# Performance work log

Measured on AMD Instinct MI355X. Metric: run time of the kernel, lower is better.

Reference implementation:

```python
import jax, jax.numpy as jnp
import numpy as np
from jax import lax

# Dims (match init_kwargs)
NP, DP = 32, 8      # num_primary_a, dim_primary_a
NT, DT = 16, 16     # num_timecaps_a, dim_timecaps
KT = 3              # kernel_timecaps_a
EPS = 1e-7


def setup_inputs() -> dict:
    key = jax.random.key(0)
    k1, k2, k3 = jax.random.split(key, 3)
    B, T = 8, 1024
    x = jax.random.normal(k1, (B, T, NP, DP), dtype=jnp.float32)
    # Conv2D kernel: HWIO = [kernel_t, dim_primary_a, in_ch=1, out_ch=NT*DT]
    conv_kernel = jax.random.normal(k2, (KT, DP, 1, NT * DT), dtype=jnp.float32) * 0.05
    conv_bias = jnp.zeros((NT * DT,), dtype=jnp.float32)
    B_weight = jax.random.normal(k3, (T, NT, 1, NP), dtype=jnp.float32) * 0.05
    return {"x": x, "conv_kernel": conv_kernel, "conv_bias": conv_bias, "B_weight": B_weight}


def reference(x, conv_kernel, conv_bias, B_weight):
    B, T, Np, Dp = x.shape
    # reshape1: [B, T, Np*Dp, 1]
    xr = x.reshape(B, T, Np * Dp, 1)
    # Conv2D(filters=NT*DT, kernel=[KT, Dp], strides=[1, Dp], padding='same', relu)
    y = lax.conv_general_dilated(
        xr, conv_kernel,
        window_strides=(1, Dp), padding='SAME',
        dimension_numbers=('NHWC', 'HWIO', 'NHWC'))
    y = jax.nn.relu(y + conv_bias)  # [B, T, Np, NT*DT]
    # reshape2 + permute -> U_hat: [B, T, NT, Np, DT]
    U = y.reshape(B, T, Np, NT, DT).transpose(0, 1, 3, 2, 4)
    # self-similarity attention
    A = jnp.einsum('btnpd,btnqd->btnpq', U, U) / jnp.sqrt(jnp.float32(Dp))
    C = jax.nn.softmax(A.sum(axis=-2, keepdims=True), axis=-1)  # [B,T,NT,1,Np]
    out = jnp.einsum('btnop,btnpd->btnod', C + B_weight, U)  # [B,T,NT,1,DT]
    out = out[..., 0, :]  # squeeze axis=-2 -> [B,T,NT,DT]
    # squash
    norm = jnp.linalg.norm(out, axis=-1, keepdims=True)
    sq = norm * norm
    return (sq / (sq + 1.0)) * (out / (norm + EPS))
```

## Files before the change

### kernel.cpp

```cpp
#include <hip/hip_runtime.h>

#define T_DIM 1024

typedef short short8 __attribute__((ext_vector_type(8)));
typedef float f32x4  __attribute__((ext_vector_type(4)));

__device__ __forceinline__ unsigned pk_bf16(float lo, float hi) {
    unsigned r;
    asm("v_cvt_pk_bf16_f32 %0, %1, %2" : "=v"(r) : "v"(lo), "v"(hi));
    return r;
}

__global__ void kpack_kernel(const float* __restrict__ K, uint4* __restrict__ Kp) {
    const int kb  = blockIdx.x;
    const int col = threadIdx.x;
    uint4 wv = make_uint4(0u, 0u, 0u, 0u);
    if (kb < 3) {
        const float* kp = K + kb * 8 * 256 + col;
        wv.x = pk_bf16(kp[0 * 256], kp[1 * 256]);
        wv.y = pk_bf16(kp[2 * 256], kp[3 * 256]);
        wv.z = pk_bf16(kp[4 * 256], kp[5 * 256]);
        wv.w = pk_bf16(kp[6 * 256], kp[7 * 256]);
    }
    Kp[kb * 256 + col] = wv;
}

__device__ __forceinline__ void allred_add16_x4(float& a, float& b, float& c, float& d) {
    asm volatile(
        "s_nop 1\n\t"
        "v_add_f32_dpp %0,%0,%0 row_ror:8 row_mask:0xf bank_mask:0xf\n\t"
        "v_add_f32_dpp %1,%1,%1 row_ror:8 row_mask:0xf bank_mask:0xf\n\t"
        "v_add_f32_dpp %2,%2,%2 row_ror:8 row_mask:0xf bank_mask:0xf\n\t"
        "v_add_f32_dpp %3,%3,%3 row_ror:8 row_mask:0xf bank_mask:0xf\n\t"
        "v_add_f32_dpp %0,%0,%0 row_ror:4 row_mask:0xf bank_mask:0xf\n\t"
        "v_add_f32_dpp %1,%1,%1 row_ror:4 row_mask:0xf bank_mask:0xf\n\t"
        "v_add_f32_dpp %2,%2,%2 row_ror:4 row_mask:0xf bank_mask:0xf\n\t"
        "v_add_f32_dpp %3,%3,%3 row_ror:4 row_mask:0xf bank_mask:0xf\n\t"
        "v_add_f32_dpp %0,%0,%0 row_ror:2 row_mask:0xf bank_mask:0xf\n\t"
        "v_add_f32_dpp %1,%1,%1 row_ror:2 row_mask:0xf bank_mask:0xf\n\t"
        "v_add_f32_dpp %2,%2,%2 row_ror:2 row_mask:0xf bank_mask:0xf\n\t"
        "v_add_f32_dpp %3,%3,%3 row_ror:2 row_mask:0xf bank_mask:0xf\n\t"
        "v_add_f32_dpp %0,%0,%0 row_ror:1 row_mask:0xf bank_mask:0xf\n\t"
        "v_add_f32_dpp %1,%1,%1 row_ror:1 row_mask:0xf bank_mask:0xf\n\t"
        "v_add_f32_dpp %2,%2,%2 row_ror:1 row_mask:0xf bank_mask:0xf\n\t"
        "v_add_f32_dpp %3,%3,%3 row_ror:1 row_mask:0xf bank_mask:0xf"
        : "+v"(a), "+v"(b), "+v"(c), "+v"(d));
}
__device__ __forceinline__ void allred_add16_v4(f32x4& v) {
    float a = v[0], b = v[1], c = v[2], d = v[3];
    allred_add16_x4(a, b, c, d);
    v = (f32x4){a, b, c, d};
}
__device__ __forceinline__ float allred_add16_s(float v) {
    asm volatile(
        "s_nop 1\n\t"
        "v_add_f32_dpp %0,%0,%0 row_ror:8 row_mask:0xf bank_mask:0xf\n\t"
        "s_nop 1\n\t"
        "v_add_f32_dpp %0,%0,%0 row_ror:4 row_mask:0xf bank_mask:0xf\n\t"
        "s_nop 1\n\t"
        "v_add_f32_dpp %0,%0,%0 row_ror:2 row_mask:0xf bank_mask:0xf\n\t"
        "s_nop 1\n\t"
        "v_add_f32_dpp %0,%0,%0 row_ror:1 row_mask:0xf bank_mask:0xf"
        : "+v"(v));
    return v;
}

__device__ __forceinline__ void wave_ds_fence() {
    asm volatile("s_waitcnt lgkmcnt(0)" ::: "memory");
}

__device__ __forceinline__ int uidx(int q, int o) {
    return q * 256 + ((((o >> 2) ^ (q & 7)) << 2) | (o & 3));
}

__global__ __launch_bounds__(256, 5) void caps_kernel(
    const float* __restrict__ x,
    const float* __restrict__ Bw,
    const uint4* __restrict__ Kp,
    const float* __restrict__ bias,
    float* __restrict__ out)
{
    const int bt  = blockIdx.x;
    const int t   = bt & (T_DIM - 1);
    const int tid = threadIdx.x;
    const int l   = tid & 63;
    const int w   = tid >> 6;
    const int kb  = l >> 4;
    const int r16 = l & 15;

    __shared__ float Urow[32 * 256];

    const int n = tid >> 4, j = tid & 15;
    const float bwj0 = Bw[(size_t)t * 512 + n * 32 + j];
    const float bwj1 = Bw[(size_t)t * 512 + n * 32 + 16 + j];

    const int  tt    = t + kb - 1;
    const bool valid = (kb < 3) && (tt >= 0) && (tt < T_DIM);
    short8 bx[2];
    #pragma unroll
    for (int qt = 0; qt < 2; ++qt) {
        float4 x0 = make_float4(0.f, 0.f, 0.f, 0.f), x1 = x0;
        if (valid) {
            const float* xp = x + ((size_t)(bt + kb - 1) * 256 + (qt * 16 + r16) * 8);
            x0 = *reinterpret_cast<const float4*>(xp);
            x1 = *reinterpret_cast<const float4*>(xp + 4);
        }
        union { short8 s; uint4 u; } bu;
        bu.u.x = pk_bf16(x0.x, x0.y);
        bu.u.y = pk_bf16(x0.z, x0.w);
        bu.u.z = pk_bf16(x1.x, x1.y);
        bu.u.w = pk_bf16(x1.z, x1.w);
        bx[qt] = bu.s;
    }

    short8 af[4];
    f32x4  bo4[4];
    #pragma unroll
    for (int oti = 0; oti < 4; ++oti) {
        union { short8 s; uint4 u; } au;
        au.u = Kp[kb * 256 + w * 64 + oti * 16 + r16];
        af[oti] = au.s;
        const float4 b4 = *reinterpret_cast<const float4*>(
            &bias[w * 64 + oti * 16 + kb * 4]);
        bo4[oti] = (f32x4){b4.x, b4.y, b4.z, b4.w};
    }

    f32x4 acc[2][4];
    #pragma unroll
    for (int qt = 0; qt < 2; ++qt)
        #pragma unroll
        for (int oti = 0; oti < 4; ++oti)
            acc[qt][oti] = __builtin_amdgcn_mfma_f32_16x16x32_bf16(
                af[oti], bx[qt], bo4[oti], 0, 0, 0);

    #pragma unroll
    for (int qt = 0; qt < 2; ++qt) {
        const int q = qt * 16 + r16;
        #pragma unroll
        for (int oti = 0; oti < 4; ++oti) {
            const int obase = w * 64 + oti * 16 + kb * 4;
            f32x4 uv;
            #pragma unroll
            for (int e = 0; e < 4; ++e)
                uv[e] = fmaxf(acc[qt][oti][e], 0.f);
            *reinterpret_cast<f32x4*>(&Urow[uidx(q, obase)]) = uv;
        }
    }

    wave_ds_fence();

    f32x4 r0[4], r1[4];
    #pragma unroll
    for (int i = 0; i < 4; ++i) {
        r0[i] = *reinterpret_cast<const f32x4*>(&Urow[uidx(j,      n * 16 + 4 * i)]);
        r1[i] = *reinterpret_cast<const f32x4*>(&Urow[uidx(j + 16, n * 16 + 4 * i)]);
    }
    asm volatile("" : "+v"(r0[0]), "+v"(r0[1]), "+v"(r0[2]), "+v"(r0[3]),
                      "+v"(r1[0]), "+v"(r1[1]), "+v"(r1[2]), "+v"(r1[3]));

    f32x4 V[4];
    #pragma unroll
    for (int i = 0; i < 4; ++i) {
        V[i] = r0[i] + r1[i];
        allred_add16_v4(V[i]);
    }

    float s0 = 0.f, s1 = 0.f;
    #pragma unroll
    for (int i = 0; i < 4; ++i)
        #pragma unroll
        for (int c = 0; c < 4; ++c) {
            s0 = fmaf(V[i][c], r0[i][c], s0);
            s1 = fmaf(V[i][c], r1[i][c], s1);
        }
    const float is8 = 0.35355339059327373f;
    s0 *= is8;
    s1 *= is8;

    const float e0 = __expf(s0), e1 = __expf(s1);
    const float es = allred_add16_s(e0 + e1);
    const float inv = __builtin_amdgcn_rcpf(es);

    const float c0 = fmaf(e0, inv, bwj0);
    const float c1 = fmaf(e1, inv, bwj1);

    f32x4 op[4];
    #pragma unroll
    for (int i = 0; i < 4; ++i) {
        #pragma unroll
        for (int c = 0; c < 4; ++c)
            op[i][c] = fmaf(c0, r0[i][c], c1 * r1[i][c]);
        allred_add16_v4(op[i]);
    }

    float ss = 0.f;
    #pragma unroll
    for (int i = 0; i < 4; ++i)
        #pragma unroll
        for (int c = 0; c < 4; ++c) ss = fmaf(op[i][c], op[i][c], ss);

    float csel[4];
    #pragma unroll
    for (int i = 0; i < 4; ++i) {
        const float lo = (j & 1) ? op[i][1] : op[i][0];
        const float hi = (j & 1) ? op[i][3] : op[i][2];
        csel[i] = (j & 2) ? hi : lo;
    }
    const float oxa = (j & 4) ? csel[1] : csel[0];
    const float oxb = (j & 4) ? csel[3] : csel[2];
    const float ox  = (j & 8) ? oxb : oxa;

    const float nrm = sqrtf(ss);
    const float res = ss * __builtin_amdgcn_rcpf(ss + 1.f) *
                      (ox * __builtin_amdgcn_rcpf(nrm + 1e-7f));

    out[(size_t)bt * 256 + tid] = res;
}

extern "C" void kernel_launch(void* const* d_in, const int* in_sizes, int n_in,
                              void* d_out, int out_size, void* d_ws, size_t ws_size,
                              hipStream_t stream) {
    const float* x    = (const float*)d_in[0];
    const float* K    = (const float*)d_in[1];
    const float* bias = (const float*)d_in[2];
    const float* Bw   = (const float*)d_in[3];
    float* out        = (float*)d_out;
    uint4* Kp         = (uint4*)d_ws;

    kpack_kernel<<<4, 256, 0, stream>>>(K, Kp);

    const int B  = in_sizes[0] / (T_DIM * 32 * 8);
    const int nb = B * T_DIM;
    caps_kernel<<<nb, 256, 0, stream>>>(x, Bw, Kp, bias, out);
}
```

Before: 34.14 us.

## Process two timesteps per block with bf16 LDS staging and bias folded into MFMA

Each block now handles two consecutive timesteps, halving the grid, reusing the packed weight fragments and sharing adjacent x rows across both steps. The conv bias moves into the unused fourth k-block of the MFMA by pairing it with a constant-one input, so the separate bias load goes away. The U tile is stored in LDS as bf16 instead of fp32, which halves LDS traffic and footprint. In exchange U is rounded to bf16 before the attention and squash steps, which costs accuracy, and each thread now holds more registers.

```diff
diff --git a/kernel.cpp b/kernel.cpp
--- a/kernel.cpp
+++ b/kernel.cpp
@@ -11,7 +11,9 @@
     return r;
 }
 
-__global__ void kpack_kernel(const float* __restrict__ K, uint4* __restrict__ Kp) {
+__global__ void kpack_kernel(const float* __restrict__ K,
+                             const float* __restrict__ bias,
+                             uint4* __restrict__ Kp) {
     const int kb  = blockIdx.x;
     const int col = threadIdx.x;
     uint4 wv = make_uint4(0u, 0u, 0u, 0u);
@@ -21,6 +23,8 @@
         wv.y = pk_bf16(kp[2 * 256], kp[3 * 256]);
         wv.z = pk_bf16(kp[4 * 256], kp[5 * 256]);
         wv.w = pk_bf16(kp[6 * 256], kp[7 * 256]);
+    } else {
+        wv.x = pk_bf16(bias[col], 0.f);
     }
     Kp[kb * 256 + col] = wv;
 }
@@ -69,69 +73,84 @@
     asm volatile("s_waitcnt lgkmcnt(0)" ::: "memory");
 }
 
-__device__ __forceinline__ int uidx(int q, int o) {
-    return q * 256 + ((((o >> 2) ^ (q & 7)) << 2) | (o & 3));
-}
+__device__ __forceinline__ int sidx(int q, int o) {
+    return q * 256 + ((((o >> 2) ^ (q & 15)) << 2) | (o & 3));
+}
+__device__ __forceinline__ float bf_lo(unsigned u) { return __uint_as_float(u << 16); }
+__device__ __forceinline__ float bf_hi(unsigned u) { return __uint_as_float(u & 0xffff0000u); }
 
 __global__ __launch_bounds__(256, 5) void caps_kernel(
     const float* __restrict__ x,
     const float* __restrict__ Bw,
     const uint4* __restrict__ Kp,
-    const float* __restrict__ bias,
     float* __restrict__ out)
 {
-    const int bt  = blockIdx.x;
-    const int t   = bt & (T_DIM - 1);
+    const int bt2 = blockIdx.x;
+    const int b   = bt2 >> 9;
+    const int t0  = (bt2 & 511) << 1;
+    const int bt0 = (b << 10) + t0;
     const int tid = threadIdx.x;
     const int l   = tid & 63;
     const int w   = tid >> 6;
     const int kb  = l >> 4;
     const int r16 = l & 15;
-
-    __shared__ float Urow[32 * 256];
-
-    const int n = tid >> 4, j = tid & 15;
-    const float bwj0 = Bw[(size_t)t * 512 + n * 32 + j];
-    const float bwj1 = Bw[(size_t)t * 512 + n * 32 + 16 + j];
-
-    const int  tt    = t + kb - 1;
-    const bool valid = (kb < 3) && (tt >= 0) && (tt < T_DIM);
-    short8 bx[2];
-    #pragma unroll
-    for (int qt = 0; qt < 2; ++qt) {
-        float4 x0 = make_float4(0.f, 0.f, 0.f, 0.f), x1 = x0;
-        if (valid) {
-            const float* xp = x + ((size_t)(bt + kb - 1) * 256 + (qt * 16 + r16) * 8);
-            x0 = *reinterpret_cast<const float4*>(xp);
-            x1 = *reinterpret_cast<const float4*>(xp + 4);
-        }
-        union { short8 s; uint4 u; } bu;
-        bu.u.x = pk_bf16(x0.x, x0.y);
-        bu.u.y = pk_bf16(x0.z, x0.w);
-        bu.u.z = pk_bf16(x1.x, x1.y);
-        bu.u.w = pk_bf16(x1.z, x1.w);
-        bx[qt] = bu.s;
+    const int n   = tid >> 4, j = tid & 15;
+
+    __shared__ unsigned short U16[2][32 * 256];
+
+    const float* bwp = Bw + (size_t)t0 * 512 + n * 32 + j;
+    const float bw00 = bwp[0],   bw01 = bwp[16];
+    const float bw10 = bwp[512], bw11 = bwp[528];
+
+    short8 bxA[2], bxB[2];
+    if (kb == 3) {
+        union { short8 s; uint4 u; } one;
+        one.u = make_uint4(0x00003F80u, 0u, 0u, 0u);
+        bxA[0] = bxA[1] = bxB[0] = bxB[1] = one.s;
+    } else {
+        const bool validA = (t0 - 1 + kb) >= 0;
+        const bool validB = (t0 + kb) < T_DIM;
+        const float* xrow = x + ((size_t)(bt0 + kb - 1)) * 256;
+        #pragma unroll
+        for (int qt = 0; qt < 2; ++qt) {
+            const float* pA = xrow + (qt * 16 + r16) * 8;
+            float4 a0 = make_float4(0.f, 0.f, 0.f, 0.f), a1 = a0;
+            float4 b0 = a0, b1 = a0;
+            if (validA) {
+                a0 = *reinterpret_cast<const float4*>(pA);
+                a1 = *reinterpret_cast<const float4*>(pA + 4);
+            }
+            if (validB) {
+                b0 = *reinterpret_cast<const float4*>(pA + 256);
+                b1 = *reinterpret_cast<const float4*>(pA + 260);
+            }
+            union { short8 s; uint4 u; } ua, ub;
+            ua.u.x = pk_bf16(a0.x, a0.y);  ua.u.y = pk_bf16(a0.z, a0.w);
+            ua.u.z = pk_bf16(a1.x, a1.y);  ua.u.w = pk_bf16(a1.z, a1.w);
+            ub.u.x = pk_bf16(b0.x, b0.y);  ub.u.y = pk_bf16(b0.z, b0.w);
+            ub.u.z = pk_bf16(b1.x, b1.y);  ub.u.w = pk_bf16(b1.z, b1.w);
+            bxA[qt] = ua.s;
+            bxB[qt] = ub.s;
+        }
     }
 
     short8 af[4];
-    f32x4  bo4[4];
     #pragma unroll
     for (int oti = 0; oti < 4; ++oti) {
         union { short8 s; uint4 u; } au;
         au.u = Kp[kb * 256 + w * 64 + oti * 16 + r16];
         af[oti] = au.s;
-        const float4 b4 = *reinterpret_cast<const float4*>(
-            &bias[w * 64 + oti * 16 + kb * 4]);
-        bo4[oti] = (f32x4){b4.x, b4.y, b4.z, b4.w};
-    }
-
-    f32x4 acc[2][4];
+    }
+
+    const f32x4 z = (f32x4){0.f, 0.f, 0.f, 0.f};
+    f32x4 acc0[2][4], acc1[2][4];
     #pragma unroll
     for (int qt = 0; qt < 2; ++qt)
         #pragma unroll
-        for (int oti = 0; oti < 4; ++oti)
-            acc[qt][oti] = __builtin_amdgcn_mfma_f32_16x16x32_bf16(
-                af[oti], bx[qt], bo4[oti], 0, 0, 0);
+        for (int oti = 0; oti < 4; ++oti) {
+            acc0[qt][oti] = __builtin_amdgcn_mfma_f32_16x16x32_bf16(af[oti], bxA[qt], z, 0, 0, 0);
+            acc1[qt][oti] = __builtin_amdgcn_mfma_f32_16x16x32_bf16(af[oti], bxB[qt], z, 0, 0, 0);
+        }
 
     #pragma unroll
     for (int qt = 0; qt < 2; ++qt) {
@@ -139,82 +158,90 @@
         #pragma unroll
         for (int oti = 0; oti < 4; ++oti) {
             const int obase = w * 64 + oti * 16 + kb * 4;
-            f32x4 uv;
+            uint2 p0, p1;
+            p0.x = pk_bf16(fmaxf(acc0[qt][oti][0], 0.f), fmaxf(acc0[qt][oti][1], 0.f));
+            p0.y = pk_bf16(fmaxf(acc0[qt][oti][2], 0.f), fmaxf(acc0[qt][oti][3], 0.f));
+            p1.x = pk_bf16(fmaxf(acc1[qt][oti][0], 0.f), fmaxf(acc1[qt][oti][1], 0.f));
+            p1.y = pk_bf16(fmaxf(acc1[qt][oti][2], 0.f), fmaxf(acc1[qt][oti][3], 0.f));
+            *reinterpret_cast<uint2*>(&U16[0][sidx(q, obase)]) = p0;
+            *reinterpret_cast<uint2*>(&U16[1][sidx(q, obase)]) = p1;
+        }
+    }
+
+    wave_ds_fence();
+
+    #pragma unroll
+    for (int ti = 0; ti < 2; ++ti) {
+        const unsigned short* Ub = U16[ti];
+        const float bwj0 = ti ? bw10 : bw00;
+        const float bwj1 = ti ? bw11 : bw01;
+
+        f32x4 r0[4], r1[4];
+        #pragma unroll
+        for (int i = 0; i < 4; ++i) {
+            const uint2 a = *reinterpret_cast<const uint2*>(&Ub[sidx(j,      n * 16 + 4 * i)]);
+            const uint2 c = *reinterpret_cast<const uint2*>(&Ub[sidx(j + 16, n * 16 + 4 * i)]);
+            r0[i] = (f32x4){bf_lo(a.x), bf_hi(a.x), bf_lo(a.y), bf_hi(a.y)};
+            r1[i] = (f32x4){bf_lo(c.x), bf_hi(c.x), bf_lo(c.y), bf_hi(c.y)};
+        }
+
+        f32x4 V[4];
+        #pragma unroll
+        for (int i = 0; i < 4; ++i) {
+            V[i] = r0[i] + r1[i];
+            allred_add16_v4(V[i]);
+        }
+
+        float s0 = 0.f, s1 = 0.f;
+        #pragma unroll
+        for (int i = 0; i < 4; ++i)
             #pragma unroll
-            for (int e = 0; e < 4; ++e)
-                uv[e] = fmaxf(acc[qt][oti][e], 0.f);
-            *reinterpret_cast<f32x4*>(&Urow[uidx(q, obase)]) = uv;
-        }
-    }
-
-    wave_ds_fence();
-
-    f32x4 r0[4], r1[4];
-    #pragma unroll
-    for (int i = 0; i < 4; ++i) {
-        r0[i] = *reinterpret_cast<const f32x4*>(&Urow[uidx(j,      n * 16 + 4 * i)]);
-        r1[i] = *reinterpret_cast<const f32x4*>(&Urow[uidx(j + 16, n * 16 + 4 * i)]);
-    }
-    asm volatile("" : "+v"(r0[0]), "+v"(r0[1]), "+v"(r0[2]), "+v"(r0[3]),
-                      "+v"(r1[0]), "+v"(r1[1]), "+v"(r1[2]), "+v"(r1[3]));
-
-    f32x4 V[4];
-    #pragma unroll
-    for (int i = 0; i < 4; ++i) {
-        V[i] = r0[i] + r1[i];
-        allred_add16_v4(V[i]);
-    }
-
-    float s0 = 0.f, s1 = 0.f;
-    #pragma unroll
-    for (int i = 0; i < 4; ++i)
-        #pragma unroll
-        for (int c = 0; c < 4; ++c) {
-            s0 = fmaf(V[i][c], r0[i][c], s0);
-            s1 = fmaf(V[i][c], r1[i][c], s1);
-        }
-    const float is8 = 0.35355339059327373f;
-    s0 *= is8;
-    s1 *= is8;
-
-    const float e0 = __expf(s0), e1 = __expf(s1);
-    const float es = allred_add16_s(e0 + e1);
-    const float inv = __builtin_amdgcn_rcpf(es);
-
-    const float c0 = fmaf(e0, inv, bwj0);
-    const float c1 = fmaf(e1, inv, bwj1);
-
-    f32x4 op[4];
-    #pragma unroll
-    for (int i = 0; i < 4; ++i) {
-        #pragma unroll
-        for (int c = 0; c < 4; ++c)
-            op[i][c] = fmaf(c0, r0[i][c], c1 * r1[i][c]);
-        allred_add16_v4(op[i]);
-    }
-
-    float ss = 0.f;
-    #pragma unroll
-    for (int i = 0; i < 4; ++i)
-        #pragma unroll
-        for (int c = 0; c < 4; ++c) ss = fmaf(op[i][c], op[i][c], ss);
-
-    float csel[4];
-    #pragma unroll
-    for (int i = 0; i < 4; ++i) {
-        const float lo = (j & 1) ? op[i][1] : op[i][0];
-        const float hi = (j & 1) ? op[i][3] : op[i][2];
-        csel[i] = (j & 2) ? hi : lo;
-    }
-    const float oxa = (j & 4) ? csel[1] : csel[0];
-    const float oxb = (j & 4) ? csel[3] : csel[2];
-    const float ox  = (j & 8) ? oxb : oxa;
-
-    const float nrm = sqrtf(ss);
-    const float res = ss * __builtin_amdgcn_rcpf(ss + 1.f) *
-                      (ox * __builtin_amdgcn_rcpf(nrm + 1e-7f));
-
-    out[(size_t)bt * 256 + tid] = res;
+            for (int c = 0; c < 4; ++c) {
+                s0 = fmaf(V[i][c], r0[i][c], s0);
+                s1 = fmaf(V[i][c], r1[i][c], s1);
+            }
+        const float is8 = 0.35355339059327373f;
+        s0 *= is8;
+        s1 *= is8;
+
+        const float e0 = __expf(s0), e1 = __expf(s1);
+        const float es = allred_add16_s(e0 + e1);
+        const float inv = __builtin_amdgcn_rcpf(es);
+        const float c0 = fmaf(e0, inv, bwj0);
+        const float c1 = fmaf(e1, inv, bwj1);
+
+        f32x4 op[4];
+        #pragma unroll
+        for (int i = 0; i < 4; ++i) {
+            #pragma unroll
+            for (int c = 0; c < 4; ++c)
+                op[i][c] = fmaf(c0, r0[i][c], c1 * r1[i][c]);
+            allred_add16_v4(op[i]);
+        }
+
+        float ss = 0.f;
+        #pragma unroll
+        for (int i = 0; i < 4; ++i)
+            #pragma unroll
+            for (int c = 0; c < 4; ++c) ss = fmaf(op[i][c], op[i][c], ss);
+
+        float csel[4];
+        #pragma unroll
+        for (int i = 0; i < 4; ++i) {
+            const float lo = (j & 1) ? op[i][1] : op[i][0];
+            const float hi = (j & 1) ? op[i][3] : op[i][2];
+            csel[i] = (j & 2) ? hi : lo;
+        }
+        const float oxa = (j & 4) ? csel[1] : csel[0];
+        const float oxb = (j & 4) ? csel[3] : csel[2];
+        const float ox  = (j & 8) ? oxb : oxa;
+
+        const float nrm = sqrtf(ss);
+        const float res = ss * __builtin_amdgcn_rcpf(ss + 1.f) *
+                          (ox * __builtin_amdgcn_rcpf(nrm + 1e-7f));
+
+        out[(size_t)(bt0 + ti) * 256 + tid] = res;
+    }
 }
 
 extern "C" void kernel_launch(void* const* d_in, const int* in_sizes, int n_in,
@@ -227,9 +254,9 @@
     float* out        = (float*)d_out;
     uint4* Kp         = (uint4*)d_ws;
 
-    kpack_kernel<<<4, 256, 0, stream>>>(K, Kp);
+    kpack_kernel<<<4, 256, 0, stream>>>(K, bias, Kp);
 
     const int B  = in_sizes[0] / (T_DIM * 32 * 8);
-    const int nb = B * T_DIM;
-    caps_kernel<<<nb, 256, 0, stream>>>(x, Bw, Kp, bias, out);
-}
+    const int nb = B * (T_DIM / 2);
+    caps_kernel<<<nb, 256, 0, stream>>>(x, Bw, Kp, out);
+}
```

New measurement: 34.41 us. Within noise of the previous version (+0.8%).

## Fold bias into MFMA, pad LDS rows, replace output allreduce with swizzle reduce-scatter

Applied to the files above, without the earlier changes.

Packs the conv bias into the unused fourth K-block of the packed weights and feeds a constant-one input lane, so the MFMA adds the bias and the per-thread bias loads go away. The XOR-swizzled LDS layout is replaced by a padded row stride of 260 floats. The 16-wide output allreduce (64 DPP adds) becomes a recursive-halving reduce-scatter using ds_swizzle, followed by a single scalar allreduce for the norm. It also switches exp to exp2 with a folded constant and lowers the launch-bounds occupancy hint from 5 to 4. The larger LDS footprint and ds_swizzle latency may offset the savings in ALU work.

```diff
diff --git a/kernel.cpp b/kernel.cpp
--- a/kernel.cpp
+++ b/kernel.cpp
@@ -11,7 +11,9 @@
     return r;
 }
 
-__global__ void kpack_kernel(const float* __restrict__ K, uint4* __restrict__ Kp) {
+__global__ void kpack_kernel(const float* __restrict__ K,
+                             const float* __restrict__ bias,
+                             uint4* __restrict__ Kp) {
     const int kb  = blockIdx.x;
     const int col = threadIdx.x;
     uint4 wv = make_uint4(0u, 0u, 0u, 0u);
@@ -21,6 +23,8 @@
         wv.y = pk_bf16(kp[2 * 256], kp[3 * 256]);
         wv.z = pk_bf16(kp[4 * 256], kp[5 * 256]);
         wv.w = pk_bf16(kp[6 * 256], kp[7 * 256]);
+    } else {
+        wv.x = pk_bf16(bias[col], 0.f);
     }
     Kp[kb * 256 + col] = wv;
 }
@@ -69,15 +73,17 @@
     asm volatile("s_waitcnt lgkmcnt(0)" ::: "memory");
 }
 
-__device__ __forceinline__ int uidx(int q, int o) {
-    return q * 256 + ((((o >> 2) ^ (q & 7)) << 2) | (o & 3));
-}
-
-__global__ __launch_bounds__(256, 5) void caps_kernel(
+template <int CODE>
+__device__ __forceinline__ float swz_xor(float v) {
+    return __int_as_float(__builtin_amdgcn_ds_swizzle(__float_as_int(v), CODE));
+}
+
+#define USTRIDE 260
+
+__global__ __launch_bounds__(256, 4) void caps_kernel(
     const float* __restrict__ x,
     const float* __restrict__ Bw,
     const uint4* __restrict__ Kp,
-    const float* __restrict__ bias,
     float* __restrict__ out)
 {
     const int bt  = blockIdx.x;
@@ -87,76 +93,76 @@
     const int w   = tid >> 6;
     const int kb  = l >> 4;
     const int r16 = l & 15;
-
-    __shared__ float Urow[32 * 256];
-
-    const int n = tid >> 4, j = tid & 15;
+    const int n   = tid >> 4, j = tid & 15;
+
+    __shared__ float Urow[32 * USTRIDE];
+
     const float bwj0 = Bw[(size_t)t * 512 + n * 32 + j];
     const float bwj1 = Bw[(size_t)t * 512 + n * 32 + 16 + j];
 
-    const int  tt    = t + kb - 1;
-    const bool valid = (kb < 3) && (tt >= 0) && (tt < T_DIM);
     short8 bx[2];
-    #pragma unroll
-    for (int qt = 0; qt < 2; ++qt) {
-        float4 x0 = make_float4(0.f, 0.f, 0.f, 0.f), x1 = x0;
-        if (valid) {
-            const float* xp = x + ((size_t)(bt + kb - 1) * 256 + (qt * 16 + r16) * 8);
-            x0 = *reinterpret_cast<const float4*>(xp);
-            x1 = *reinterpret_cast<const float4*>(xp + 4);
+    if (kb == 3) {
+        union { short8 s; uint4 u; } one;
+        one.u = make_uint4(0x00003F80u, 0u, 0u, 0u);
+        bx[0] = bx[1] = one.s;
+    } else {
+        const int  tt    = t + kb - 1;
+        const bool valid = (tt >= 0) && (tt < T_DIM);
+        #pragma unroll
+        for (int qt = 0; qt < 2; ++qt) {
+            float4 x0 = make_float4(0.f, 0.f, 0.f, 0.f), x1 = x0;
+            if (valid) {
+                const float* xp = x + ((size_t)(bt + kb - 1) * 256 + (qt * 16 + r16) * 8);
+                x0 = *reinterpret_cast<const float4*>(xp);
+                x1 = *reinterpret_cast<const float4*>(xp + 4);
+            }
+            union { short8 s; uint4 u; } bu;
+            bu.u.x = pk_bf16(x0.x, x0.y);
+            bu.u.y = pk_bf16(x0.z, x0.w);
+            bu.u.z = pk_bf16(x1.x, x1.y);
+            bu.u.w = pk_bf16(x1.z, x1.w);
+            bx[qt] = bu.s;
         }
-        union { short8 s; uint4 u; } bu;
-        bu.u.x = pk_bf16(x0.x, x0.y);
-        bu.u.y = pk_bf16(x0.z, x0.w);
-        bu.u.z = pk_bf16(x1.x, x1.y);
-        bu.u.w = pk_bf16(x1.z, x1.w);
-        bx[qt] = bu.s;
     }
 
     short8 af[4];
-    f32x4  bo4[4];
     #pragma unroll
     for (int oti = 0; oti < 4; ++oti) {
         union { short8 s; uint4 u; } au;
         au.u = Kp[kb * 256 + w * 64 + oti * 16 + r16];
         af[oti] = au.s;
-        const float4 b4 = *reinterpret_cast<const float4*>(
-            &bias[w * 64 + oti * 16 + kb * 4]);
-        bo4[oti] = (f32x4){b4.x, b4.y, b4.z, b4.w};
-    }
-
+    }
+
+    const f32x4 z = (f32x4){0.f, 0.f, 0.f, 0.f};
     f32x4 acc[2][4];
     #pragma unroll
     for (int qt = 0; qt < 2; ++qt)
         #pragma unroll
         for (int oti = 0; oti < 4; ++oti)
             acc[qt][oti] = __builtin_amdgcn_mfma_f32_16x16x32_bf16(
-                af[oti], bx[qt], bo4[oti], 0, 0, 0);
-
-    #pragma unroll
-    for (int qt = 0; qt < 2; ++qt) {
-        const int q = qt * 16 + r16;
+                af[oti], bx[qt], z, 0, 0, 0);
+
+    float* wbase = &Urow[r16 * USTRIDE + w * 64 + kb * 4];
+    #pragma unroll
+    for (int qt = 0; qt < 2; ++qt)
         #pragma unroll
         for (int oti = 0; oti < 4; ++oti) {
-            const int obase = w * 64 + oti * 16 + kb * 4;
             f32x4 uv;
             #pragma unroll
             for (int e = 0; e < 4; ++e)
                 uv[e] = fmaxf(acc[qt][oti][e], 0.f);
-            *reinterpret_cast<f32x4*>(&Urow[uidx(q, obase)]) = uv;
+            *reinterpret_cast<f32x4*>(&wbase[qt * 16 * USTRIDE + oti * 16]) = uv;
         }
-    }
 
     wave_ds_fence();
 
+    const float* rbase = &Urow[j * USTRIDE + n * 16];
     f32x4 r0[4], r1[4];
     #pragma unroll
     for (int i = 0; i < 4; ++i) {
-        r0[i] = *reinterpret_cast<const f32x4*>(&Urow[uidx(j,      n * 16 + 4 * i)]);
-        r1[i] = *reinterpret_cast<const f32x4*>(&Urow[uidx(j + 16, n * 16 + 4 * i)]);
-    }
-    asm volatile("" : "+v"(r0[0]), "+v"(r0[1]), "+v"(r0[2]), "+v"(r0[3]),
-                      "+v"(r1[0]), "+v"(r1[1]), "+v"(r1[2]), "+v"(r1[3]));
+        r0[i] = *reinterpret_cast<const f32x4*>(&rbase[4 * i]);
+        r1[i] = *reinterpret_cast<const f32x4*>(&rbase[16 * USTRIDE + 4 * i]);
+    }
 
     f32x4 V[4];
     #pragma unroll
@@ -173,43 +179,49 @@
             s0 = fmaf(V[i][c], r0[i][c], s0);
             s1 = fmaf(V[i][c], r1[i][c], s1);
         }
-    const float is8 = 0.35355339059327373f;
-    s0 *= is8;
-    s1 *= is8;
-
-    const float e0 = __expf(s0), e1 = __expf(s1);
+
+    const float C2 = 0.51011597846f;
+    const float e0 = exp2f(s0 * C2), e1 = exp2f(s1 * C2);
     const float es = allred_add16_s(e0 + e1);
     const float inv = __builtin_amdgcn_rcpf(es);
-
     const float c0 = fmaf(e0, inv, bwj0);
     const float c1 = fmaf(e1, inv, bwj1);
 
-    f32x4 op[4];
-    #pragma unroll
-    for (int i = 0; i < 4; ++i) {
+    float op16[16];
+    #pragma unroll
+    for (int i = 0; i < 4; ++i)
         #pragma unroll
         for (int c = 0; c < 4; ++c)
-            op[i][c] = fmaf(c0, r0[i][c], c1 * r1[i][c]);
-        allred_add16_v4(op[i]);
-    }
-
-    float ss = 0.f;
-    #pragma unroll
-    for (int i = 0; i < 4; ++i)
-        #pragma unroll
-        for (int c = 0; c < 4; ++c) ss = fmaf(op[i][c], op[i][c], ss);
-
-    float csel[4];
-    #pragma unroll
-    for (int i = 0; i < 4; ++i) {
-        const float lo = (j & 1) ? op[i][1] : op[i][0];
-        const float hi = (j & 1) ? op[i][3] : op[i][2];
-        csel[i] = (j & 2) ? hi : lo;
-    }
-    const float oxa = (j & 4) ? csel[1] : csel[0];
-    const float oxb = (j & 4) ? csel[3] : csel[2];
-    const float ox  = (j & 8) ? oxb : oxa;
-
+            op16[4 * i + c] = fmaf(c0, r0[i][c], c1 * r1[i][c]);
+
+    float v8[8];
+    #pragma unroll
+    for (int s = 0; s < 8; ++s) {
+        const float keep = (j & 8) ? op16[s + 8] : op16[s];
+        const float send = (j & 8) ? op16[s] : op16[s + 8];
+        v8[s] = keep + swz_xor<0x201F>(send);
+    }
+    float v4[4];
+    #pragma unroll
+    for (int s = 0; s < 4; ++s) {
+        const float keep = (j & 4) ? v4[0] * 0.f + ((j & 4) ? v8[s + 4] : v8[s]) : v8[s];
+        (void)keep;
+        const float kp = (j & 4) ? v8[s + 4] : v8[s];
+        const float sd = (j & 4) ? v8[s] : v8[s + 4];
+        v4[s] = kp + swz_xor<0x101F>(sd);
+    }
+    float v2[2];
+    #pragma unroll
+    for (int s = 0; s < 2; ++s) {
+        const float kp = (j & 2) ? v4[s + 2] : v4[s];
+        const float sd = (j & 2) ? v4[s] : v4[s + 2];
+        v2[s] = kp + swz_xor<0x081F>(sd);
+    }
+    const float kp1 = (j & 1) ? v2[1] : v2[0];
+    const float sd1 = (j & 1) ? v2[0] : v2[1];
+    const float ox = kp1 + swz_xor<0x041F>(sd1);
+
+    const float ss  = allred_add16_s(ox * ox);
     const float nrm = sqrtf(ss);
     const float res = ss * __builtin_amdgcn_rcpf(ss + 1.f) *
                       (ox * __builtin_amdgcn_rcpf(nrm + 1e-7f));
@@ -227,9 +239,9 @@
     float* out        = (float*)d_out;
     uint4* Kp         = (uint4*)d_ws;
 
-    kpack_kernel<<<4, 256, 0, stream>>>(K, Kp);
+    kpack_kernel<<<4, 256, 0, stream>>>(K, bias, Kp);
 
     const int B  = in_sizes[0] / (T_DIM * 32 * 8);
     const int nb = B * T_DIM;
-    caps_kernel<<<nb, 256, 0, stream>>>(x, Bw, Kp, bias, out);
-}
+    caps_kernel<<<nb, 256, 0, stream>>>(x, Bw, Kp, out);
+}
```

New measurement: 33.81 us. About the same (-1.0%).
